# Kernel tuning notes

Hardware: AMD Instinct MI355X
Metric: run time of the kernel (lower is better)

The kernel has to match this reference:

```python
import jax, jax.numpy as jnp
import numpy as np

B, T, E = 32, 100, 512
H = 640          # predictor embed/hidden dim
J = 640          # joint hidden dim
V = 4096         # vocab size; blank index == V
BLANK = V
MAX_SYMBOLS = 2  # max_symbols_per_step


def setup_inputs() -> dict:
    key = jax.random.key(0)
    ks = jax.random.split(key, 11)
    s = 0.02
    return {
        "encoder_output": jax.random.normal(ks[0], (B, E, T), jnp.float32),
        "encoded_lengths": jax.random.randint(ks[1], (B,), 0, T).astype(jnp.int32),
        "embed": jax.random.normal(ks[2], (V + 1, H), jnp.float32) * s,
        "W_i": jax.random.normal(ks[3], (H, 4 * H), jnp.float32) * s,
        "W_h": jax.random.normal(ks[4], (H, 4 * H), jnp.float32) * s,
        "b_lstm": jnp.zeros((4 * H,), jnp.float32),
        "W_enc": jax.random.normal(ks[5], (E, J), jnp.float32) * s,
        "W_pred": jax.random.normal(ks[6], (H, J), jnp.float32) * s,
        "b_joint": jnp.zeros((J,), jnp.float32),
        "W_out": jax.random.normal(ks[7], (J, V + 1), jnp.float32) * s,
        "b_out": jnp.zeros((V + 1,), jnp.float32),
    }


def _lstm_step(x, h, c, W_i, W_h, b):
    z = x @ W_i + h @ W_h + b                      # [B, 4H]
    i, f, g, o = jnp.split(z, 4, axis=-1)
    i, f, o = jax.nn.sigmoid(i), jax.nn.sigmoid(f), jax.nn.sigmoid(o)
    c = f * c + i * jnp.tanh(g)
    return o * jnp.tanh(c), c


def _greedy_decode(enc_bte, lengths, embed, W_i, W_h, b_lstm,
                   W_enc, W_pred, b_joint, W_out, b_out):
    """Batched RNNT greedy decode. Returns (labels [B,T*MS], counts [B], score [B]).
    Instead of the host-side early break when blank_mask is all-true, we run the
    bounded inner loop with per-sequence commit masking; once a sequence is blank
    its state/label/output freeze, so the per-sequence results are identical."""
    Bv = enc_bte.shape[0]
    enc_proj = enc_bte @ W_enc                     # [B, T, J] (same math as per-step enc projection)
    batch_ix = jnp.arange(Bv)

    h0 = jnp.zeros((Bv, H), enc_bte.dtype)
    c0 = jnp.zeros((Bv, H), enc_bte.dtype)
    last0 = jnp.full((Bv,), BLANK, jnp.int32)      # SOS == blank
    labels0 = jnp.full((Bv, T * MAX_SYMBOLS), BLANK, jnp.int32)
    counts0 = jnp.zeros((Bv,), jnp.int32)
    score0 = jnp.zeros((Bv,), jnp.float32)

    def inner(icarry, s_and_t):
        h, c, last_label, blank_mask, labels, counts, score = icarry
        s, t = s_and_t
        use_sos = jnp.logical_and(t == 0, s == 0)
        x = jnp.where(use_sos, 0.0, embed[last_label])      # [B, H]; SOS -> zero vector
        h1, c1 = _lstm_step(x, h, c, W_i, W_h, b_lstm)
        logits = jax.nn.relu(enc_proj[:, t] + h1 @ W_pred + b_joint) @ W_out + b_out  # [B, V+1]
        logp = jax.nn.log_softmax(logits, axis=-1)          # CPU path in original
        k = jnp.argmax(logp, axis=-1)                       # [B]
        v = jnp.take_along_axis(logp, k[:, None], axis=-1)[:, 0]
        new_blank = blank_mask | (k == BLANK)
        commit = ~new_blank                                  # only non-blank sequences advance
        cm = commit[:, None]
        h = jnp.where(cm, h1, h)
        c = jnp.where(cm, c1, c)
        k32 = k.astype(jnp.int32)
        last_label = jnp.where(commit, k32, last_label)
        labels = labels.at[batch_ix, counts].set(
            jnp.where(commit, k32, labels[batch_ix, counts]))
        counts = counts + commit.astype(jnp.int32)
        score = score + jnp.where(commit, v, 0.0)
        return (h, c, last_label, new_blank, labels, counts, score), None

    def outer(carry, t):
        h, c, last_label, labels, counts, score = carry
        blank_mask = t >= lengths                            # [B]
        icarry = (h, c, last_label, blank_mask, labels, counts, score)
        icarry, _ = jax.lax.scan(
            lambda cc, s: inner(cc, (s, t)), icarry, jnp.arange(MAX_SYMBOLS))
        h, c, last_label, _, labels, counts, score = icarry
        return (h, c, last_label, labels, counts, score), None

    carry = (h0, c0, last0, labels0, counts0, score0)
    carry, _ = jax.lax.scan(outer, carry, jnp.arange(T))
    _, _, _, labels, counts, score = carry
    return labels, counts, score


def reference(encoder_output, encoded_lengths, embed, W_i, W_h, b_lstm,
              W_enc, W_pred, b_joint, W_out, b_out):
    enc = jnp.transpose(encoder_output, (0, 2, 1))           # (B, F, T) -> (B, T, F)
    labels, counts, score = _greedy_decode(
        enc, encoded_lengths, embed, W_i, W_h, b_lstm,
        W_enc, W_pred, b_joint, W_out, b_out)
    return labels, counts, score
```

## Files before the change

kernel.cpp:

```cpp
#include <hip/hip_runtime.h>


#define NB 512
#define S1B 320
#define HRS 20480
#define ARRS 64
#define GOS 256

__device__ __forceinline__ unsigned f2ord(float f) {
  unsigned u = __float_as_uint(f);
  return (u & 0x80000000u) ? ~u : (u | 0x80000000u);
}
__device__ __forceinline__ float ord2f(unsigned u) {
  return __uint_as_float((u & 0x80000000u) ? (u & 0x7fffffffu) : ~u);
}
__device__ __forceinline__ unsigned long long shfl_xor_u64(unsigned long long x, int m) {
  int lo = __shfl_xor((int)(unsigned)x, m, 64);
  int hi = __shfl_xor((int)(unsigned)(x >> 32), m, 64);
  return ((unsigned long long)(unsigned)hi << 32) | (unsigned)lo;
}

__device__ __forceinline__ void st_coh_f32(float* p, float v) {
  asm volatile("global_store_dword %0, %1, off sc0 sc1" :: "v"(p), "v"(v) : "memory");
}
__device__ __forceinline__ void st_coh_u32(unsigned* p, unsigned v) {
  asm volatile("global_store_dword %0, %1, off sc0 sc1" :: "v"(p), "v"(v) : "memory");
}
__device__ __forceinline__ unsigned ld_coh_u32(const unsigned* p) {
  unsigned r;
  asm volatile("global_load_dword %0, %1, off sc0 sc1\n\ts_waitcnt vmcnt(0)"
               : "=v"(r) : "v"(p) : "memory");
  return r;
}
__device__ __forceinline__ bool poll2(const unsigned* p1, const unsigned* p2,
                                      unsigned it) {
  unsigned r1, r2;
  asm volatile("global_load_dword %0, %2, off sc0 sc1\n\t"
               "global_load_dword %1, %3, off sc0 sc1\n\t"
               "s_waitcnt vmcnt(0)"
               : "=v"(r1), "=v"(r2) : "v"(p1), "v"(p2) : "memory");
  return (r1 >= it) && (r2 >= it);
}

__device__ __forceinline__ void gbarrier(unsigned* __restrict__ arrive,
                                         unsigned* __restrict__ go, unsigned it) {
  const int blk = blockIdx.x, tid = threadIdx.x;
  __syncthreads();
  if (blk == 0) {
    int f1 = 1 + tid; if (f1 > 511) f1 = 511;
    int f2 = 257 + tid; if (f2 > 511) f2 = 511;
    while (!poll2(arrive + f1 * ARRS, arrive + f2 * ARRS, it))
      __builtin_amdgcn_s_sleep(8);
    __syncthreads();
    if (tid < 64) st_coh_u32(go + tid * GOS, it);
    __syncthreads();
  } else {
    if (tid == 0) {
      st_coh_u32(arrive + blk * ARRS, it);
      while (ld_coh_u32(go + (blk & 63) * GOS) < it) __builtin_amdgcn_s_sleep(32);
    }
    __syncthreads();
  }
}

__device__ __forceinline__ float4 tile_read(const float (*__restrict__ t)[160],
                                            int b, int c) {
  return *(const float4*)&t[b][(c ^ (b & 7)) << 2];
}

__global__ __launch_bounds__(256) void rnnt_prep(
    const float* __restrict__ enc, const float* __restrict__ W_i,
    const float* __restrict__ W_h, const float* __restrict__ W_pred,
    const float* __restrict__ W_out, const float* __restrict__ W_enc,
    const float* __restrict__ b_joint,
    float* __restrict__ out, float* __restrict__ Wcat_t,
    float* __restrict__ Wpred_t, float* __restrict__ Wout_t,
    float* __restrict__ enc_projB, float* __restrict__ h_ring,
    unsigned long long* __restrict__ kslot, unsigned long long* __restrict__ sslot,
    unsigned* __restrict__ arrive, unsigned* __restrict__ go) {
  const int blk = blockIdx.x, tid = threadIdx.x;
  const int gtid = blk * 256 + tid;
  const int GT = gridDim.x * 256;
  __shared__ float s_tr[32][33];

  for (int x = gtid; x < 6464; x += GT) out[x] = (x < 6400) ? 4096.0f : 0.0f;
  for (int x = gtid; x < HRS; x += GT) h_ring[(size_t)200 * HRS + x] = 0.f;
  for (int x = gtid; x < 51200; x += GT) { kslot[x] = 0ull; sslot[x] = 0ull; }
  for (int x = gtid; x < NB * ARRS; x += GT) arrive[x] = 0u;
  for (int x = gtid; x < 64 * GOS; x += GT) go[x] = 0u;

  {
    const int NT0 = 1600, NT1 = 1600, NT2 = 400, NT3 = 2580;
    for (int tl = blk; tl < NT0 + NT1 + NT2 + NT3; tl += gridDim.x) {
      const float* src; float* dst; int C, DS, DO, CT; int tt = tl;
      if (tt < NT0)               { src = W_i;    dst = Wcat_t;  C = 2560; DS = 1280; DO = 0;   CT = 80; }
      else if ((tt -= NT0) < NT1) { src = W_h;    dst = Wcat_t;  C = 2560; DS = 1280; DO = 640; CT = 80; }
      else if ((tt -= NT1) < NT2) { src = W_pred; dst = Wpred_t; C = 640;  DS = 640;  DO = 0;   CT = 20; }
      else { tt -= NT2;             src = W_out;  dst = Wout_t;  C = 4097; DS = 640;  DO = 0;   CT = 129; }
      int rt = tt / CT, ct = tt % CT;
      int r0 = rt * 32, c0 = ct * 32;
      __syncthreads();
#pragma unroll
      for (int p = 0; p < 4; ++p) {
        int rr = (tid >> 5) + 8 * p, cc = tid & 31;
        float v = 0.f;
        if (c0 + cc < C) v = src[(r0 + rr) * C + c0 + cc];
        s_tr[rr][cc] = v;
      }
      __syncthreads();
#pragma unroll
      for (int p = 0; p < 4; ++p) {
        int cc2 = (tid >> 5) + 8 * p, rr2 = tid & 31;
        if (c0 + cc2 < C) dst[(c0 + cc2) * DS + DO + r0 + rr2] = s_tr[rr2][cc2];
      }
    }
  }

  for (int idx = gtid; idx < 2048000; idx += GT) {
    int b = idx / 64000, r = idx % 64000;
    int tt = r / 640, j = r % 640;
    const float* ep = enc + b * 51200;
    float acc = b_joint[j];
#pragma unroll 4
    for (int e = 0; e < 512; ++e) acc += ep[e * 100 + tt] * W_enc[e * 640 + j];
    enc_projB[idx] = acc;
  }
}

__global__ __launch_bounds__(256, 2) void rnnt_decode(
    const int* __restrict__ lens, const float* __restrict__ embed,
    const float* __restrict__ b_lstm, const float* __restrict__ b_out,
    float* __restrict__ out,
    const float* __restrict__ Wcat_t, const float* __restrict__ Wpred_t,
    const float* __restrict__ Wout_t, const float* __restrict__ enc_projB,
    float* __restrict__ h_ring, float* __restrict__ jt_ring,
    unsigned long long* __restrict__ kslot, unsigned long long* __restrict__ sslot,
    unsigned* __restrict__ arrive, unsigned* __restrict__ go) {
  const int blk = blockIdx.x, tid = threadIdx.x;

  __shared__ float s_tile[32][160];
  __shared__ float s_wout[8 * 644];
  __shared__ float s_zp[2][4][32][2];
  __shared__ float s_red[4][64];
  __shared__ unsigned long long s_dk[32], s_ds[32];
  __shared__ int s_last[32], s_hsrc[32], s_commit[32];

  for (int x = tid; x < 8 * 160; x += 256) {
    int col = x / 160, cc = x - col * 160;
    *(float4*)&s_wout[col * 644 + cc * 4] =
        *(const float4*)(Wout_t + (size_t)(blk * 8 + col) * 640 + cc * 4);
  }

  int last_r = 4096, hsrc_r = 200, cnt_r = 0;
  bool blank_r = false;
  float score_r = 0.f;
  float c_comm = 0.f, c_cand = 0.f;
  unsigned it = 0;
  const int len_b = lens[tid & 31];
  const int rb = tid >> 3, q = tid & 7;

  for (int i = 0;; ++i) {
    if (i > 0) {
      int ip = i - 1;
      int b8 = tid >> 3, sl = tid & 7;
      unsigned long long kv = kslot[((size_t)ip * 32 + b8) * 8 + sl];
      unsigned long long sv = sslot[((size_t)ip * 32 + b8) * 8 + sl];
#pragma unroll
      for (int d = 1; d < 8; d <<= 1) {
        unsigned long long ok = shfl_xor_u64(kv, d);
        if (ok > kv) kv = ok;
        sv += shfl_xor_u64(sv, d);
      }
      if (sl == 0) { s_dk[b8] = kv; s_ds[b8] = sv; }
    }
    __syncthreads();
    if (tid < 32) {
      int b = tid;
      int cm = 0;
      if (i > 0) {
        unsigned long long key = s_dk[b], sum = s_ds[b];
        int kArg = 4096 - (int)(key & 0xffffffffu);
        float bl = ord2f((unsigned)(key >> 32));
        float lse = logf((float)sum * 0x1p-32f);
        float vsc = bl - lse;
        int im1 = i - 1, tp = im1 >> 1, sp = im1 & 1;
        bool blank_in = (sp == 0) ? (tp >= len_b) : blank_r;
        bool nb = blank_in || (kArg == 4096);
        blank_r = nb;
        if (!nb) {
          if (blk == b) out[b * 200 + cnt_r] = (float)kArg;
          last_r = kArg; hsrc_r = im1; cnt_r++; score_r += vsc; cm = 1;
        }
      }
      if (i == 200 && blk == b) { out[6400 + b] = (float)cnt_r; out[6432 + b] = score_r; }
      s_last[b] = last_r; s_hsrc[b] = hsrc_r; s_commit[b] = cm;
    }
    __syncthreads();
    if (i == 200) return;
    const int t = i >> 1;

    if (blk < S1B) {
      const int b = tid & 31;
      const int g = (tid >> 5) & 3;
      const int half = tid >> 7;
      const int j0 = blk * 2;
      float a0 = 0.f, a1 = 0.f, a2 = 0.f, a3 = 0.f;
      float e0 = 0.f, e1 = 0.f, e2 = 0.f, e3 = 0.f;
      if (i > 0) {
        float4 pf0, pf1, pf2, pf3, pf4;
        {
          const float* s0 = embed + (size_t)s_last[rb] * 640;
          pf0 = *(const float4*)(s0 + (q << 2));
          pf1 = *(const float4*)(s0 + ((q + 8) << 2));
          pf2 = *(const float4*)(s0 + ((q + 16) << 2));
          pf3 = *(const float4*)(s0 + ((q + 24) << 2));
          pf4 = *(const float4*)(s0 + ((q + 32) << 2));
        }
#pragma unroll 1
        for (int tt = 0; tt < 8; ++tt) {
          *(float4*)&s_tile[rb][((q)      ^ (rb & 7)) << 2] = pf0;
          *(float4*)&s_tile[rb][((q + 8)  ^ (rb & 7)) << 2] = pf1;
          *(float4*)&s_tile[rb][((q + 16) ^ (rb & 7)) << 2] = pf2;
          *(float4*)&s_tile[rb][((q + 24) ^ (rb & 7)) << 2] = pf3;
          *(float4*)&s_tile[rb][((q + 32) ^ (rb & 7)) << 2] = pf4;
          if (tt < 7) {
            const float* src = (tt + 1 < 4)
                ? embed + (size_t)s_last[rb] * 640 + (tt + 1) * 160
                : h_ring + (size_t)s_hsrc[rb] * HRS + rb * 640 + (tt - 3) * 160;
            pf0 = *(const float4*)(src + (q << 2));
            pf1 = *(const float4*)(src + ((q + 8) << 2));
            pf2 = *(const float4*)(src + ((q + 16) << 2));
            pf3 = *(const float4*)(src + ((q + 24) << 2));
            pf4 = *(const float4*)(src + ((q + 32) << 2));
          }
          __syncthreads();
          if ((tt >> 2) == half) {
            const float* wr = Wcat_t + (size_t)(g * 640 + j0) * 1280 +
                              half * 640 + (tt & 3) * 160;
            const float* wr2 = wr + 1280;
#pragma unroll 8
            for (int cc = 0; cc < 40; ++cc) {
              float4 xv = tile_read(s_tile, b, cc);
              float4 wa = *(const float4*)(wr + cc * 4);
              float4 wb = *(const float4*)(wr2 + cc * 4);
              a0 += wa.x * xv.x; a1 += wa.y * xv.y;
              a2 += wa.z * xv.z; a3 += wa.w * xv.w;
              e0 += wb.x * xv.x; e1 += wb.y * xv.y;
              e2 += wb.z * xv.z; e3 += wb.w * xv.w;
            }
          }
          __syncthreads();
        }
      }
      float z0 = (a0 + a1) + (a2 + a3);
      float z1 = (e0 + e1) + (e2 + e3);
      if (half == 0) { z0 += b_lstm[g * 640 + j0]; z1 += b_lstm[g * 640 + j0 + 1]; }
      s_zp[half][g][b][0] = z0;
      s_zp[half][g][b][1] = z1;
    }
    __syncthreads();
    if (blk < S1B && tid < 64) {
      const int b = tid >> 1, j_l = tid & 1;
      float zi = s_zp[0][0][b][j_l] + s_zp[1][0][b][j_l];
      float zf = s_zp[0][1][b][j_l] + s_zp[1][1][b][j_l];
      float zg = s_zp[0][2][b][j_l] + s_zp[1][2][b][j_l];
      float zo = s_zp[0][3][b][j_l] + s_zp[1][3][b][j_l];
      if (s_commit[b]) c_comm = c_cand;
      float ig = 1.f / (1.f + expf(-zi));
      float fg = 1.f / (1.f + expf(-zf));
      float og = 1.f / (1.f + expf(-zo));
      float cn = fg * c_comm + ig * tanhf(zg);
      float hn = og * tanhf(cn);
      c_cand = cn;
      st_coh_f32(&h_ring[(size_t)i * HRS + b * 640 + blk * 2 + j_l], hn);
    }
    gbarrier(arrive, go, ++it);

    if (blk < S1B) {
      const int w = tid >> 6, lane = tid & 63, bb = lane >> 1, j_l = lane & 1;
      const int j = blk * 2 + j_l;
      float r0 = 0.f, r1 = 0.f, r2 = 0.f, r3 = 0.f;
      float4 pf0, pf1, pf2, pf3, pf4;
      {
        const float* s0 = h_ring + (size_t)i * HRS + rb * 640;
        pf0 = *(const float4*)(s0 + (q << 2));
        pf1 = *(const float4*)(s0 + ((q + 8) << 2));
        pf2 = *(const float4*)(s0 + ((q + 16) << 2));
        pf3 = *(const float4*)(s0 + ((q + 24) << 2));
        pf4 = *(const float4*)(s0 + ((q + 32) << 2));
      }
#pragma unroll 1
      for (int tt = 0; tt < 4; ++tt) {
        *(float4*)&s_tile[rb][((q)      ^ (rb & 7)) << 2] = pf0;
        *(float4*)&s_tile[rb][((q + 8)  ^ (rb & 7)) << 2] = pf1;
        *(float4*)&s_tile[rb][((q + 16) ^ (rb & 7)) << 2] = pf2;
        *(float4*)&s_tile[rb][((q + 24) ^ (rb & 7)) << 2] = pf3;
        *(float4*)&s_tile[rb][((q + 32) ^ (rb & 7)) << 2] = pf4;
        if (tt < 3) {
          const float* src = h_ring + (size_t)i * HRS + rb * 640 + (tt + 1) * 160;
          pf0 = *(const float4*)(src + (q << 2));
          pf1 = *(const float4*)(src + ((q + 8) << 2));
          pf2 = *(const float4*)(src + ((q + 16) << 2));
          pf3 = *(const float4*)(src + ((q + 24) << 2));
          pf4 = *(const float4*)(src + ((q + 32) << 2));
        }
        __syncthreads();
        if (w == tt) {
          const float* wp = Wpred_t + (size_t)j * 640 + w * 160;
#pragma unroll 8
          for (int cc = 0; cc < 40; ++cc) {
            float4 hv = tile_read(s_tile, bb, cc);
            float4 wv = *(const float4*)(wp + cc * 4);
            r0 += wv.x * hv.x; r1 += wv.y * hv.y;
            r2 += wv.z * hv.z; r3 += wv.w * hv.w;
          }
        }
        __syncthreads();
      }
      s_red[w][lane] = (r0 + r1) + (r2 + r3);
    }
    __syncthreads();
    if (blk < S1B && tid < 64) {
      const int b = tid >> 1, j_l = tid & 1, j = blk * 2 + j_l;
      float sm = (s_red[0][tid] + s_red[1][tid]) + (s_red[2][tid] + s_red[3][tid]);
      float val = enc_projB[(b * 100 + t) * 640 + j] + sm;
      st_coh_f32(&jt_ring[(size_t)i * HRS + b * 640 + j], fmaxf(val, 0.f));
    }
    gbarrier(arrive, go, ++it);

    {
      const int b = tid >> 3, v_l = tid & 7;
      const int v = blk * 8 + v_l;
      const int kq = v_l;
      float a0 = 0.f, a1 = 0.f, a2 = 0.f, a3 = 0.f;
      float p0 = 0.f, p1 = 0.f, p2 = 0.f, p3 = 0.f;
      float4 pf0, pf1, pf2, pf3, pf4;
      {
        const float* s0 = jt_ring + (size_t)i * HRS + rb * 640;
        pf0 = *(const float4*)(s0 + (q << 2));
        pf1 = *(const float4*)(s0 + ((q + 8) << 2));
        pf2 = *(const float4*)(s0 + ((q + 16) << 2));
        pf3 = *(const float4*)(s0 + ((q + 24) << 2));
        pf4 = *(const float4*)(s0 + ((q + 32) << 2));
      }
#pragma unroll 1
      for (int tt = 0; tt < 4; ++tt) {
        *(float4*)&s_tile[rb][((q)      ^ (rb & 7)) << 2] = pf0;
        *(float4*)&s_tile[rb][((q + 8)  ^ (rb & 7)) << 2] = pf1;
        *(float4*)&s_tile[rb][((q + 16) ^ (rb & 7)) << 2] = pf2;
        *(float4*)&s_tile[rb][((q + 24) ^ (rb & 7)) << 2] = pf3;
        *(float4*)&s_tile[rb][((q + 32) ^ (rb & 7)) << 2] = pf4;
        if (tt < 3) {
          const float* src = jt_ring + (size_t)i * HRS + rb * 640 + (tt + 1) * 160;
          pf0 = *(const float4*)(src + (q << 2));
          pf1 = *(const float4*)(src + ((q + 8) << 2));
          pf2 = *(const float4*)(src + ((q + 16) << 2));
          pf3 = *(const float4*)(src + ((q + 24) << 2));
          pf4 = *(const float4*)(src + ((q + 32) << 2));
        }
        __syncthreads();
        const float* wk = s_wout + v_l * 644 + tt * 160;
#pragma unroll 8
        for (int cc = 0; cc < 40; ++cc) {
          float4 jv = tile_read(s_tile, b, cc);
          float4 wv = *(const float4*)(wk + cc * 4);
          a0 += wv.x * jv.x; a1 += wv.y * jv.y;
          a2 += wv.z * jv.z; a3 += wv.w * jv.w;
        }
        if (blk == NB - 1 && (kq >> 1) == tt) {
          const float* wb4 = Wout_t + (size_t)4096 * 640 + kq * 80;
          const int c0 = (kq & 1) * 20;
#pragma unroll
          for (int cc = 0; cc < 20; ++cc) {
            float4 jv = tile_read(s_tile, b, c0 + cc);
            float4 wv = *(const float4*)(wb4 + cc * 4);
            p0 += wv.x * jv.x; p1 += wv.y * jv.y;
            p2 += wv.z * jv.z; p3 += wv.w * jv.w;
          }
        }
        __syncthreads();
      }
      float acc = ((a0 + a1) + (a2 + a3)) + b_out[v];
      unsigned long long key =
          ((unsigned long long)f2ord(acc) << 32) | (unsigned)(4096 - v);
      unsigned long long isum =
          (unsigned long long)(expf(acc) * 4294967296.0f + 0.5f);
#pragma unroll
      for (int d = 1; d < 8; d <<= 1) {
        unsigned long long ok = shfl_xor_u64(key, d);
        if (ok > key) key = ok;
        isum += shfl_xor_u64(isum, d);
      }
      if (v_l == 0) {
        atomicMax(&kslot[((size_t)i * 32 + b) * 8 + (blk & 7)], key);
        atomicAdd(&sslot[((size_t)i * 32 + b) * 8 + (blk & 7)], isum);
      }
      if (blk == NB - 1) {
        float part = (p0 + p1) + (p2 + p3);
#pragma unroll
        for (int d = 1; d < 8; d <<= 1) part += __shfl_xor(part, d, 64);
        if (kq == 0) {
          float aB = part + b_out[4096];
          unsigned long long key2 = ((unsigned long long)f2ord(aB) << 32);
          unsigned long long is2 =
              (unsigned long long)(expf(aB) * 4294967296.0f + 0.5f);
          atomicMax(&kslot[((size_t)i * 32 + b) * 8 + 7], key2);
          atomicAdd(&sslot[((size_t)i * 32 + b) * 8 + 7], is2);
        }
      }
    }
    gbarrier(arrive, go, ++it);
  }
}

extern "C" void kernel_launch(void* const* d_in, const int* in_sizes, int n_in,
                              void* d_out, int out_size, void* d_ws, size_t ws_size,
                              hipStream_t stream) {
  (void)in_sizes; (void)n_in; (void)out_size; (void)ws_size;
  const float* enc    = (const float*)d_in[0];
  const int*   lens   = (const int*)d_in[1];
  const float* embed  = (const float*)d_in[2];
  const float* W_i    = (const float*)d_in[3];
  const float* W_h    = (const float*)d_in[4];
  const float* b_lstm = (const float*)d_in[5];
  const float* W_enc  = (const float*)d_in[6];
  const float* W_pred = (const float*)d_in[7];
  const float* b_joint= (const float*)d_in[8];
  const float* W_out  = (const float*)d_in[9];
  const float* b_out  = (const float*)d_in[10];
  float* out = (float*)d_out;

  char* ws = (char*)d_ws;
  size_t off = 0;
  auto carve = [&](size_t bytes) -> void* {
    void* p = ws + off;
    off += (bytes + 255) & ~(size_t)255;
    return p;
  };
  unsigned* arrive           = (unsigned*)carve((size_t)NB * ARRS * 4);
  unsigned* go               = (unsigned*)carve((size_t)64 * GOS * 4);
  unsigned long long* kslot  = (unsigned long long*)carve((size_t)51200 * 8);
  unsigned long long* sslot  = (unsigned long long*)carve((size_t)51200 * 8);
  float* h_ring   = (float*)carve((size_t)201 * HRS * 4);
  float* jt_ring  = (float*)carve((size_t)200 * HRS * 4);
  float* Wpred_t  = (float*)carve((size_t)640 * 640 * 4);
  float* Wcat_t   = (float*)carve((size_t)2560 * 1280 * 4);
  float* Wout_t   = (float*)carve((size_t)4097 * 640 * 4);
  float* enc_projB= (float*)carve((size_t)32 * 100 * 640 * 4);

  rnnt_prep<<<2048, 256, 0, stream>>>(
      enc, W_i, W_h, W_pred, W_out, W_enc, b_joint,
      out, Wcat_t, Wpred_t, Wout_t, enc_projB, h_ring, kslot, sslot, arrive, go);
  rnnt_decode<<<NB, 256, 0, stream>>>(
      lens, embed, b_lstm, b_out, out,
      Wcat_t, Wpred_t, Wout_t, enc_projB, h_ring, jt_ring, kslot, sslot,
      arrive, go);
}
```

Measured before the change: 12.93 ms.

## Replace all-block grid barriers with per-stage counting semaphores

Swaps the centralized arrive/go grid barrier for per-iteration, per-stage atomic counters, split over 8 slots. Blocks that do the LSTM stage wait only on the other 320 LSTM blocks, and the vocab blocks wait only for the joint-hidden stage and the previous argmax reduction. The aim is to cut barrier round-trip latency and to stop the 192 idle blocks from joining the LSTM and joint-hidden barriers. In exchange there are extra coherent read-backs after stores and atomics, a much larger semaphore array, and correctness now rests on the ordering of those read-backs.

```diff
diff --git a/kernel.cpp b/kernel.cpp
--- a/kernel.cpp
+++ b/kernel.cpp
@@ -4,8 +4,7 @@
 #define NB 512
 #define S1B 320
 #define HRS 20480
-#define ARRS 64
-#define GOS 256
+#define SEMOFF(p, i) ((((p) * 201) + (i)) << 9)
 
 __device__ __forceinline__ unsigned f2ord(float f) {
   unsigned u = __float_as_uint(f);
@@ -21,9 +20,6 @@
 }
 
 __device__ __forceinline__ void st_coh_f32(float* p, float v) {
-  asm volatile("global_store_dword %0, %1, off sc0 sc1" :: "v"(p), "v"(v) : "memory");
-}
-__device__ __forceinline__ void st_coh_u32(unsigned* p, unsigned v) {
   asm volatile("global_store_dword %0, %1, off sc0 sc1" :: "v"(p), "v"(v) : "memory");
 }
 __device__ __forceinline__ unsigned ld_coh_u32(const unsigned* p) {
@@ -32,35 +28,30 @@
                : "=v"(r) : "v"(p) : "memory");
   return r;
 }
-__device__ __forceinline__ bool poll2(const unsigned* p1, const unsigned* p2,
-                                      unsigned it) {
-  unsigned r1, r2;
-  asm volatile("global_load_dword %0, %2, off sc0 sc1\n\t"
-               "global_load_dword %1, %3, off sc0 sc1\n\t"
-               "s_waitcnt vmcnt(0)"
-               : "=v"(r1), "=v"(r2) : "v"(p1), "v"(p2) : "memory");
-  return (r1 >= it) && (r2 >= it);
-}
-
-__device__ __forceinline__ void gbarrier(unsigned* __restrict__ arrive,
-                                         unsigned* __restrict__ go, unsigned it) {
-  const int blk = blockIdx.x, tid = threadIdx.x;
+__device__ __forceinline__ void rb_coh(const void* p) {
+  unsigned r;
+  asm volatile("global_load_dword %0, %1, off sc0 sc1\n\ts_waitcnt vmcnt(0)"
+               : "=v"(r) : "v"(p) : "memory");
+  (void)r;
+}
+
+__device__ __forceinline__ void sem_wait(const unsigned* __restrict__ semPI,
+                                         unsigned target) {
+  if (threadIdx.x < 8) {
+    const unsigned* p = semPI + threadIdx.x * 64;
+    for (;;) {
+      unsigned v = ld_coh_u32(p);
+      v += __shfl_xor(v, 1, 64);
+      v += __shfl_xor(v, 2, 64);
+      v += __shfl_xor(v, 4, 64);
+      if (v >= target) break;
+      __builtin_amdgcn_s_sleep(8);
+    }
+  }
   __syncthreads();
-  if (blk == 0) {
-    int f1 = 1 + tid; if (f1 > 511) f1 = 511;
-    int f2 = 257 + tid; if (f2 > 511) f2 = 511;
-    while (!poll2(arrive + f1 * ARRS, arrive + f2 * ARRS, it))
-      __builtin_amdgcn_s_sleep(8);
-    __syncthreads();
-    if (tid < 64) st_coh_u32(go + tid * GOS, it);
-    __syncthreads();
-  } else {
-    if (tid == 0) {
-      st_coh_u32(arrive + blk * ARRS, it);
-      while (ld_coh_u32(go + (blk & 63) * GOS) < it) __builtin_amdgcn_s_sleep(32);
-    }
-    __syncthreads();
-  }
+}
+__device__ __forceinline__ void sem_bump(unsigned* __restrict__ semPI, int blk) {
+  atomicAdd(semPI + (blk & 7) * 64, 1u);
 }
 
 __device__ __forceinline__ float4 tile_read(const float (*__restrict__ t)[160],
@@ -77,7 +68,7 @@
     float* __restrict__ Wpred_t, float* __restrict__ Wout_t,
     float* __restrict__ enc_projB, float* __restrict__ h_ring,
     unsigned long long* __restrict__ kslot, unsigned long long* __restrict__ sslot,
-    unsigned* __restrict__ arrive, unsigned* __restrict__ go) {
+    unsigned* __restrict__ sem) {
   const int blk = blockIdx.x, tid = threadIdx.x;
   const int gtid = blk * 256 + tid;
   const int GT = gridDim.x * 256;
@@ -86,8 +77,7 @@
   for (int x = gtid; x < 6464; x += GT) out[x] = (x < 6400) ? 4096.0f : 0.0f;
   for (int x = gtid; x < HRS; x += GT) h_ring[(size_t)200 * HRS + x] = 0.f;
   for (int x = gtid; x < 51200; x += GT) { kslot[x] = 0ull; sslot[x] = 0ull; }
-  for (int x = gtid; x < NB * ARRS; x += GT) arrive[x] = 0u;
-  for (int x = gtid; x < 64 * GOS; x += GT) go[x] = 0u;
+  for (int x = gtid; x < 3 * 201 * 512; x += GT) sem[x] = 0u;
 
   {
     const int NT0 = 1600, NT1 = 1600, NT2 = 400, NT3 = 2580;
@@ -135,7 +125,7 @@
     const float* __restrict__ Wout_t, const float* __restrict__ enc_projB,
     float* __restrict__ h_ring, float* __restrict__ jt_ring,
     unsigned long long* __restrict__ kslot, unsigned long long* __restrict__ sslot,
-    unsigned* __restrict__ arrive, unsigned* __restrict__ go) {
+    unsigned* __restrict__ sem) {
   const int blk = blockIdx.x, tid = threadIdx.x;
 
   __shared__ float s_tile[32][160];
@@ -155,12 +145,12 @@
   bool blank_r = false;
   float score_r = 0.f;
   float c_comm = 0.f, c_cand = 0.f;
-  unsigned it = 0;
   const int len_b = lens[tid & 31];
   const int rb = tid >> 3, q = tid & 7;
 
   for (int i = 0;; ++i) {
     if (i > 0) {
+      sem_wait(sem + SEMOFF(2, i - 1), NB);
       int ip = i - 1;
       int b8 = tid >> 3, sl = tid & 7;
       unsigned long long kv = kslot[((size_t)ip * 32 + b8) * 8 + sl];
@@ -200,16 +190,94 @@
     const int t = i >> 1;
 
     if (blk < S1B) {
-      const int b = tid & 31;
-      const int g = (tid >> 5) & 3;
-      const int half = tid >> 7;
-      const int j0 = blk * 2;
-      float a0 = 0.f, a1 = 0.f, a2 = 0.f, a3 = 0.f;
-      float e0 = 0.f, e1 = 0.f, e2 = 0.f, e3 = 0.f;
-      if (i > 0) {
+      {
+        const int b = tid & 31;
+        const int g = (tid >> 5) & 3;
+        const int half = tid >> 7;
+        const int j0 = blk * 2;
+        float a0 = 0.f, a1 = 0.f, a2 = 0.f, a3 = 0.f;
+        float e0 = 0.f, e1 = 0.f, e2 = 0.f, e3 = 0.f;
+        if (i > 0) {
+          float4 pf0, pf1, pf2, pf3, pf4;
+          {
+            const float* s0 = embed + (size_t)s_last[rb] * 640;
+            pf0 = *(const float4*)(s0 + (q << 2));
+            pf1 = *(const float4*)(s0 + ((q + 8) << 2));
+            pf2 = *(const float4*)(s0 + ((q + 16) << 2));
+            pf3 = *(const float4*)(s0 + ((q + 24) << 2));
+            pf4 = *(const float4*)(s0 + ((q + 32) << 2));
+          }
+#pragma unroll 1
+          for (int tt = 0; tt < 8; ++tt) {
+            *(float4*)&s_tile[rb][((q)      ^ (rb & 7)) << 2] = pf0;
+            *(float4*)&s_tile[rb][((q + 8)  ^ (rb & 7)) << 2] = pf1;
+            *(float4*)&s_tile[rb][((q + 16) ^ (rb & 7)) << 2] = pf2;
+            *(float4*)&s_tile[rb][((q + 24) ^ (rb & 7)) << 2] = pf3;
+            *(float4*)&s_tile[rb][((q + 32) ^ (rb & 7)) << 2] = pf4;
+            if (tt < 7) {
+              const float* src = (tt + 1 < 4)
+                  ? embed + (size_t)s_last[rb] * 640 + (tt + 1) * 160
+                  : h_ring + (size_t)s_hsrc[rb] * HRS + rb * 640 + (tt - 3) * 160;
+              pf0 = *(const float4*)(src + (q << 2));
+              pf1 = *(const float4*)(src + ((q + 8) << 2));
+              pf2 = *(const float4*)(src + ((q + 16) << 2));
+              pf3 = *(const float4*)(src + ((q + 24) << 2));
+              pf4 = *(const float4*)(src + ((q + 32) << 2));
+            }
+            __syncthreads();
+            if ((tt >> 2) == half) {
+              const float* wr = Wcat_t + (size_t)(g * 640 + j0) * 1280 +
+                                half * 640 + (tt & 3) * 160;
+              const float* wr2 = wr + 1280;
+#pragma unroll 8
+              for (int cc = 0; cc < 40; ++cc) {
+                float4 xv = tile_read(s_tile, b, cc);
+                float4 wa = *(const float4*)(wr + cc * 4);
+                float4 wb = *(const float4*)(wr2 + cc * 4);
+                a0 += wa.x * xv.x; a1 += wa.y * xv.y;
+                a2 += wa.z * xv.z; a3 += wa.w * xv.w;
+                e0 += wb.x * xv.x; e1 += wb.y * xv.y;
+                e2 += wb.z * xv.z; e3 += wb.w * xv.w;
+              }
+            }
+            __syncthreads();
+          }
+        }
+        float z0 = (a0 + a1) + (a2 + a3);
+        float z1 = (e0 + e1) + (e2 + e3);
+        if (half == 0) { z0 += b_lstm[g * 640 + j0]; z1 += b_lstm[g * 640 + j0 + 1]; }
+        s_zp[half][g][b][0] = z0;
+        s_zp[half][g][b][1] = z1;
+      }
+      __syncthreads();
+      if (tid < 64) {
+        const int b = tid >> 1, j_l = tid & 1;
+        float zi = s_zp[0][0][b][j_l] + s_zp[1][0][b][j_l];
+        float zf = s_zp[0][1][b][j_l] + s_zp[1][1][b][j_l];
+        float zg = s_zp[0][2][b][j_l] + s_zp[1][2][b][j_l];
+        float zo = s_zp[0][3][b][j_l] + s_zp[1][3][b][j_l];
+        if (s_commit[b]) c_comm = c_cand;
+        float ig = 1.f / (1.f + expf(-zi));
+        float fg = 1.f / (1.f + expf(-zf));
+        float og = 1.f / (1.f + expf(-zo));
+        float cn = fg * c_comm + ig * tanhf(zg);
+        float hn = og * tanhf(cn);
+        c_cand = cn;
+        float* hp = &h_ring[(size_t)i * HRS + b * 640 + blk * 2 + j_l];
+        st_coh_f32(hp, hn);
+        rb_coh(hp);
+      }
+      __syncthreads();
+      if (tid == 0) sem_bump(sem + SEMOFF(0, i), blk);
+      sem_wait(sem + SEMOFF(0, i), S1B);
+
+      {
+        const int w = tid >> 6, lane = tid & 63, bb = lane >> 1, j_l = lane & 1;
+        const int j = blk * 2 + j_l;
+        float r0 = 0.f, r1 = 0.f, r2 = 0.f, r3 = 0.f;
         float4 pf0, pf1, pf2, pf3, pf4;
         {
-          const float* s0 = embed + (size_t)s_last[rb] * 640;
+          const float* s0 = h_ring + (size_t)i * HRS + rb * 640;
           pf0 = *(const float4*)(s0 + (q << 2));
           pf1 = *(const float4*)(s0 + ((q + 8) << 2));
           pf2 = *(const float4*)(s0 + ((q + 16) << 2));
@@ -217,16 +285,14 @@
           pf4 = *(const float4*)(s0 + ((q + 32) << 2));
         }
 #pragma unroll 1
-        for (int tt = 0; tt < 8; ++tt) {
+        for (int tt = 0; tt < 4; ++tt) {
           *(float4*)&s_tile[rb][((q)      ^ (rb & 7)) << 2] = pf0;
           *(float4*)&s_tile[rb][((q + 8)  ^ (rb & 7)) << 2] = pf1;
           *(float4*)&s_tile[rb][((q + 16) ^ (rb & 7)) << 2] = pf2;
           *(float4*)&s_tile[rb][((q + 24) ^ (rb & 7)) << 2] = pf3;
           *(float4*)&s_tile[rb][((q + 32) ^ (rb & 7)) << 2] = pf4;
-          if (tt < 7) {
-            const float* src = (tt + 1 < 4)
-                ? embed + (size_t)s_last[rb] * 640 + (tt + 1) * 160
-                : h_ring + (size_t)s_hsrc[rb] * HRS + rb * 640 + (tt - 3) * 160;
+          if (tt < 3) {
+            const float* src = h_ring + (size_t)i * HRS + rb * 640 + (tt + 1) * 160;
             pf0 = *(const float4*)(src + (q << 2));
             pf1 = *(const float4*)(src + ((q + 8) << 2));
             pf2 = *(const float4*)(src + ((q + 16) << 2));
@@ -234,99 +300,34 @@
             pf4 = *(const float4*)(src + ((q + 32) << 2));
           }
           __syncthreads();
-          if ((tt >> 2) == half) {
-            const float* wr = Wcat_t + (size_t)(g * 640 + j0) * 1280 +
-                              half * 640 + (tt & 3) * 160;
-            const float* wr2 = wr + 1280;
+          if (w == tt) {
+            const float* wp = Wpred_t + (size_t)j * 640 + w * 160;
 #pragma unroll 8
             for (int cc = 0; cc < 40; ++cc) {
-              float4 xv = tile_read(s_tile, b, cc);
-              float4 wa = *(const float4*)(wr + cc * 4);
-              float4 wb = *(const float4*)(wr2 + cc * 4);
-              a0 += wa.x * xv.x; a1 += wa.y * xv.y;
-              a2 += wa.z * xv.z; a3 += wa.w * xv.w;
-              e0 += wb.x * xv.x; e1 += wb.y * xv.y;
-              e2 += wb.z * xv.z; e3 += wb.w * xv.w;
+              float4 hv = tile_read(s_tile, bb, cc);
+              float4 wv = *(const float4*)(wp + cc * 4);
+              r0 += wv.x * hv.x; r1 += wv.y * hv.y;
+              r2 += wv.z * hv.z; r3 += wv.w * hv.w;
             }
           }
           __syncthreads();
         }
-      }
-      float z0 = (a0 + a1) + (a2 + a3);
-      float z1 = (e0 + e1) + (e2 + e3);
-      if (half == 0) { z0 += b_lstm[g * 640 + j0]; z1 += b_lstm[g * 640 + j0 + 1]; }
-      s_zp[half][g][b][0] = z0;
-      s_zp[half][g][b][1] = z1;
-    }
-    __syncthreads();
-    if (blk < S1B && tid < 64) {
-      const int b = tid >> 1, j_l = tid & 1;
-      float zi = s_zp[0][0][b][j_l] + s_zp[1][0][b][j_l];
-      float zf = s_zp[0][1][b][j_l] + s_zp[1][1][b][j_l];
-      float zg = s_zp[0][2][b][j_l] + s_zp[1][2][b][j_l];
-      float zo = s_zp[0][3][b][j_l] + s_zp[1][3][b][j_l];
-      if (s_commit[b]) c_comm = c_cand;
-      float ig = 1.f / (1.f + expf(-zi));
-      float fg = 1.f / (1.f + expf(-zf));
-      float og = 1.f / (1.f + expf(-zo));
-      float cn = fg * c_comm + ig * tanhf(zg);
-      float hn = og * tanhf(cn);
-      c_cand = cn;
-      st_coh_f32(&h_ring[(size_t)i * HRS + b * 640 + blk * 2 + j_l], hn);
-    }
-    gbarrier(arrive, go, ++it);
-
-    if (blk < S1B) {
-      const int w = tid >> 6, lane = tid & 63, bb = lane >> 1, j_l = lane & 1;
-      const int j = blk * 2 + j_l;
-      float r0 = 0.f, r1 = 0.f, r2 = 0.f, r3 = 0.f;
-      float4 pf0, pf1, pf2, pf3, pf4;
-      {
-        const float* s0 = h_ring + (size_t)i * HRS + rb * 640;
-        pf0 = *(const float4*)(s0 + (q << 2));
-        pf1 = *(const float4*)(s0 + ((q + 8) << 2));
-        pf2 = *(const float4*)(s0 + ((q + 16) << 2));
-        pf3 = *(const float4*)(s0 + ((q + 24) << 2));
-        pf4 = *(const float4*)(s0 + ((q + 32) << 2));
-      }
-#pragma unroll 1
-      for (int tt = 0; tt < 4; ++tt) {
-        *(float4*)&s_tile[rb][((q)      ^ (rb & 7)) << 2] = pf0;
-        *(float4*)&s_tile[rb][((q + 8)  ^ (rb & 7)) << 2] = pf1;
-        *(float4*)&s_tile[rb][((q + 16) ^ (rb & 7)) << 2] = pf2;
-        *(float4*)&s_tile[rb][((q + 24) ^ (rb & 7)) << 2] = pf3;
-        *(float4*)&s_tile[rb][((q + 32) ^ (rb & 7)) << 2] = pf4;
-        if (tt < 3) {
-          const float* src = h_ring + (size_t)i * HRS + rb * 640 + (tt + 1) * 160;
-          pf0 = *(const float4*)(src + (q << 2));
-          pf1 = *(const float4*)(src + ((q + 8) << 2));
-          pf2 = *(const float4*)(src + ((q + 16) << 2));
-          pf3 = *(const float4*)(src + ((q + 24) << 2));
-          pf4 = *(const float4*)(src + ((q + 32) << 2));
-        }
-        __syncthreads();
-        if (w == tt) {
-          const float* wp = Wpred_t + (size_t)j * 640 + w * 160;
-#pragma unroll 8
-          for (int cc = 0; cc < 40; ++cc) {
-            float4 hv = tile_read(s_tile, bb, cc);
-            float4 wv = *(const float4*)(wp + cc * 4);
-            r0 += wv.x * hv.x; r1 += wv.y * hv.y;
-            r2 += wv.z * hv.z; r3 += wv.w * hv.w;
-          }
-        }
-        __syncthreads();
-      }
-      s_red[w][lane] = (r0 + r1) + (r2 + r3);
-    }
-    __syncthreads();
-    if (blk < S1B && tid < 64) {
-      const int b = tid >> 1, j_l = tid & 1, j = blk * 2 + j_l;
-      float sm = (s_red[0][tid] + s_red[1][tid]) + (s_red[2][tid] + s_red[3][tid]);
-      float val = enc_projB[(b * 100 + t) * 640 + j] + sm;
-      st_coh_f32(&jt_ring[(size_t)i * HRS + b * 640 + j], fmaxf(val, 0.f));
-    }
-    gbarrier(arrive, go, ++it);
+        s_red[w][lane] = (r0 + r1) + (r2 + r3);
+      }
+      __syncthreads();
+      if (tid < 64) {
+        const int b = tid >> 1, j_l = tid & 1, j = blk * 2 + j_l;
+        float sm = (s_red[0][tid] + s_red[1][tid]) + (s_red[2][tid] + s_red[3][tid]);
+        float val = enc_projB[(b * 100 + t) * 640 + j] + sm;
+        float* jp = &jt_ring[(size_t)i * HRS + b * 640 + j];
+        st_coh_f32(jp, fmaxf(val, 0.f));
+        rb_coh(jp);
+      }
+      __syncthreads();
+      if (tid == 0) sem_bump(sem + SEMOFF(1, i), blk);
+    }
+
+    sem_wait(sem + SEMOFF(1, i), S1B);
 
     {
       const int b = tid >> 3, v_l = tid & 7;
@@ -392,8 +393,12 @@
         isum += shfl_xor_u64(isum, d);
       }
       if (v_l == 0) {
-        atomicMax(&kslot[((size_t)i * 32 + b) * 8 + (blk & 7)], key);
-        atomicAdd(&sslot[((size_t)i * 32 + b) * 8 + (blk & 7)], isum);
+        unsigned long long* kp = &kslot[((size_t)i * 32 + b) * 8 + (blk & 7)];
+        unsigned long long* sp = &sslot[((size_t)i * 32 + b) * 8 + (blk & 7)];
+        atomicMax(kp, key);
+        atomicAdd(sp, isum);
+        rb_coh(kp);
+        rb_coh(sp);
       }
       if (blk == NB - 1) {
         float part = (p0 + p1) + (p2 + p3);
@@ -404,12 +409,17 @@
           unsigned long long key2 = ((unsigned long long)f2ord(aB) << 32);
           unsigned long long is2 =
               (unsigned long long)(expf(aB) * 4294967296.0f + 0.5f);
-          atomicMax(&kslot[((size_t)i * 32 + b) * 8 + 7], key2);
-          atomicAdd(&sslot[((size_t)i * 32 + b) * 8 + 7], is2);
-        }
-      }
-    }
-    gbarrier(arrive, go, ++it);
+          unsigned long long* kp2 = &kslot[((size_t)i * 32 + b) * 8 + 7];
+          unsigned long long* sp2 = &sslot[((size_t)i * 32 + b) * 8 + 7];
+          atomicMax(kp2, key2);
+          atomicAdd(sp2, is2);
+          rb_coh(kp2);
+          rb_coh(sp2);
+        }
+      }
+    }
+    __syncthreads();
+    if (tid == 0) sem_bump(sem + SEMOFF(2, i), blk);
   }
 }
 
@@ -437,8 +447,7 @@
     off += (bytes + 255) & ~(size_t)255;
     return p;
   };
-  unsigned* arrive           = (unsigned*)carve((size_t)NB * ARRS * 4);
-  unsigned* go               = (unsigned*)carve((size_t)64 * GOS * 4);
+  unsigned* sem              = (unsigned*)carve((size_t)3 * 201 * 512 * 4);
   unsigned long long* kslot  = (unsigned long long*)carve((size_t)51200 * 8);
   unsigned long long* sslot  = (unsigned long long*)carve((size_t)51200 * 8);
   float* h_ring   = (float*)carve((size_t)201 * HRS * 4);
@@ -450,9 +459,8 @@
 
   rnnt_prep<<<2048, 256, 0, stream>>>(
       enc, W_i, W_h, W_pred, W_out, W_enc, b_joint,
-      out, Wcat_t, Wpred_t, Wout_t, enc_projB, h_ring, kslot, sslot, arrive, go);
+      out, Wcat_t, Wpred_t, Wout_t, enc_projB, h_ring, kslot, sslot, sem);
   rnnt_decode<<<NB, 256, 0, stream>>>(
       lens, embed, b_lstm, b_out, out,
-      Wcat_t, Wpred_t, Wout_t, enc_projB, h_ring, jt_ring, kslot, sslot,
-      arrive, go);
-}
+      Wcat_t, Wpred_t, Wout_t, enc_projB, h_ring, jt_ring, kslot, sslot, sem);
+}
```

Measured after the change: 19.11 ms. 1.48x slower.
